# Kernel tuning notes

Measured on AMD Instinct MI355X. Metric: run time of the kernel, lower is better.

## Reference

```python
import jax, jax.numpy as jnp
import numpy as np

H, W, D = 200, 200, 16          # voxel grid dims
GRID = 0.4                       # voxel size (m)
MULT = 3.0                       # scale_multiplier (3-sigma radius)
PC_MIN = np.array([-40.0, -40.0, -1.0], dtype=np.float32)
B, N, M, C = 1, 16384, 4096, 18  # batch, query points, gaussians, semantic classes


def setup_inputs() -> dict:
    key = jax.random.key(0)
    ks = jax.random.split(key, 6)
    extent = jnp.array([H, W, D], dtype=jnp.float32) * GRID
    pc_min = jnp.asarray(PC_MIN)
    # points / means strictly inside the grid so int-voxel asserts hold
    pts = pc_min + jax.random.uniform(ks[0], (B, N, 3), dtype=jnp.float32) * (extent - 1e-3)
    means3D = pc_min + jax.random.uniform(ks[1], (B, M, 3), dtype=jnp.float32) * (extent - 1e-3)
    opacities = jax.random.uniform(ks[2], (B, M), dtype=jnp.float32, minval=0.1, maxval=1.0)
    semantics = jax.random.normal(ks[3], (B, M, C), dtype=jnp.float32)
    # scales chosen so ceil(max_scale*3/0.4) >= 1 (radii assert)
    scales = jax.random.uniform(ks[4], (B, M, 3), dtype=jnp.float32, minval=0.15, maxval=0.6)
    # SPD covariance per Gaussian: diag(scales^2) + small PSD perturbation
    Bm = 0.05 * jax.random.normal(ks[5], (B, M, 3, 3), dtype=jnp.float32)
    cov3D = jnp.eye(3, dtype=jnp.float32) * (scales ** 2)[..., :, None] + Bm @ jnp.swapaxes(Bm, -1, -2)
    return {"pts": pts, "means3D": means3D, "opacities": opacities,
            "semantics": semantics, "scales": scales, "cov3D": cov3D}


def _aggregate(pts_i, means_i, op_i, sem_i, sc_i, cov_i):
    # pts_i [N,3], means_i [M,3], op_i [M], sem_i [M,C], sc_i [M,3], cov_i [M,3,3]
    pc_min = jnp.asarray(PC_MIN)
    pint = jnp.floor((pts_i - pc_min) / GRID).astype(jnp.int32)    # [N,3] voxel of each point
    mint = jnp.floor((means_i - pc_min) / GRID).astype(jnp.int32)  # [M,3] voxel of each gaussian
    radii = jnp.ceil(jnp.max(sc_i, axis=-1) * MULT / GRID).astype(jnp.int32)  # [M] voxel radius
    A = jnp.linalg.inv(cov_i)                                       # [M,3,3] conic (inverse cov)
    Am = jnp.einsum('gij,gj->gi', A, means_i)                       # [M,3]
    mAm = jnp.einsum('gi,gi->g', means_i, Am)                       # [M]
    # Mahalanobis q[n,g] = (p-m)^T A (p-m) = p^T A p - 2 p^T A m + m^T A m, via [N,9]x[9,M] GEMM
    pp = (pts_i[:, :, None] * pts_i[:, None, :]).reshape(-1, 9)     # [N,9]
    pAp = pp @ A.reshape(-1, 9).T                                   # [N,M]
    q = pAp - 2.0 * (pts_i @ Am.T) + mAm[None, :]                   # [N,M]
    # gaussian contributes to a point iff the point's voxel lies in the gaussian's radius box
    mask = jnp.all(jnp.abs(pint[:, None, :] - mint[None, :, :]) <= radii[None, :, None], axis=-1)
    w = jnp.where(mask, jnp.exp(-0.5 * q) * op_i[None, :], 0.0)     # [N,M]
    return w @ sem_i                                                # [N,C] logits


def reference(pts, means3D, opacities, semantics, scales, cov3D):
    return jax.vmap(_aggregate)(pts, means3D, opacities, semantics, scales, cov3D)
```

## Files before the change

### kernel.cpp

```cpp
#include <hip/hip_runtime.h>

namespace {
constexpr float GRIDSZ = 0.4f;
constexpr float PCXY = -40.0f;
constexpr float PCZ  = -1.0f;
constexpr int CCH = 18;
constexpr int CELLS_X = 25;
constexpr int NCELLS = CELLS_X * CELLS_X;
constexpr int VMAX = 199;
constexpr int PCAP = 128;
constexpr int GCAP = 128;
constexpr int SEMW = 20;
}

__global__ __launch_bounds__(256) void prep_kernel(
    const float* __restrict__ pts, const float* __restrict__ means,
    const float* __restrict__ scales,
    unsigned short* __restrict__ pcell, unsigned* __restrict__ gcb,
    int N, int M) {
  int id = blockIdx.x * 256 + threadIdx.x;
  if (id < M) {
    int g = id;
    float mx = means[(size_t)g * 3 + 0], my = means[(size_t)g * 3 + 1];
    int mvx = (int)floorf((mx - PCXY) / GRIDSZ);
    int mvy = (int)floorf((my - PCXY) / GRIDSZ);
    float smax = fmaxf(scales[(size_t)g * 3 + 0],
                 fmaxf(scales[(size_t)g * 3 + 1], scales[(size_t)g * 3 + 2]));
    int r = (int)ceilf(smax * 3.0f / GRIDSZ);
    int cx0 = max(mvx - r, 0) >> 3, cx1 = min(mvx + r, VMAX) >> 3;
    int cy0 = max(mvy - r, 0) >> 3, cy1 = min(mvy + r, VMAX) >> 3;
    gcb[g] = (unsigned)cx0 | ((unsigned)cx1 << 8) | ((unsigned)cy0 << 16) | ((unsigned)cy1 << 24);
  } else if (id < M + N) {
    int p = id - M;
    float px = pts[(size_t)p * 3 + 0], py = pts[(size_t)p * 3 + 1];
    int pvx = (int)floorf((px - PCXY) / GRIDSZ);
    int pvy = (int)floorf((py - PCXY) / GRIDSZ);
    pcell[p] = (unsigned short)((pvx >> 3) + CELLS_X * (pvy >> 3));
  }
}

__global__ __launch_bounds__(256) void agg_kernel(
    const float* __restrict__ pts, const float* __restrict__ means,
    const float* __restrict__ opac, const float* __restrict__ scales,
    const float* __restrict__ cov, const float* __restrict__ sem,
    const unsigned short* __restrict__ pcell, const unsigned* __restrict__ gcb,
    float* __restrict__ out, int N, int M) {
  __shared__ int pcnt_s, gcnt_s;
  __shared__ int lpi[PCAP];
  __shared__ int lvox[PCAP];
  __shared__ float4 lpts[PCAP];
  __shared__ int graw[GCAP];
  __shared__ int gsrt[GCAP];
  __shared__ int4 lbox[GCAP];
  __shared__ float4 lpay[GCAP * 3];
  __shared__ float lsem[GCAP * SEMW];
  __shared__ float buf[3][64][CCH + 1];

  const int tid = threadIdx.x, lane = tid & 63, wave = tid >> 6;
  const unsigned cellv = blockIdx.x;
  const int cx = (int)(cellv % CELLS_X), cy = (int)(cellv / CELLS_X);

  if (tid == 0) { pcnt_s = 0; gcnt_s = 0; }
  __syncthreads();

  {
    const uint4* pc4 = reinterpret_cast<const uint4*>(pcell);
    const int n8 = N >> 3;
    for (int i8 = tid; i8 < n8; i8 += 256) {
      uint4 v = pc4[i8];
      unsigned w[4] = {v.x, v.y, v.z, v.w};
#pragma unroll
      for (int k = 0; k < 4; ++k) {
        if ((w[k] & 0xFFFFu) == cellv) {
          int s = atomicAdd(&pcnt_s, 1);
          if (s < PCAP) lpi[s] = i8 * 8 + 2 * k;
        }
        if ((w[k] >> 16) == cellv) {
          int s = atomicAdd(&pcnt_s, 1);
          if (s < PCAP) lpi[s] = i8 * 8 + 2 * k + 1;
        }
      }
    }
    for (int i = (n8 << 3) + tid; i < N; i += 256) {
      if (pcell[i] == cellv) {
        int s = atomicAdd(&pcnt_s, 1);
        if (s < PCAP) lpi[s] = i;
      }
    }
  }
  {
    const uint4* gb4 = reinterpret_cast<const uint4*>(gcb);
    const int m4 = M >> 2;
    for (int i4 = tid; i4 < m4; i4 += 256) {
      uint4 v = gb4[i4];
      unsigned gk[4] = {v.x, v.y, v.z, v.w};
#pragma unroll
      for (int k = 0; k < 4; ++k) {
        unsigned pk = gk[k];
        bool hit = (cx >= (int)(pk & 255u)) & (cx <= (int)((pk >> 8) & 255u)) &
                   (cy >= (int)((pk >> 16) & 255u)) & (cy <= (int)(pk >> 24));
        if (hit) {
          int s = atomicAdd(&gcnt_s, 1);
          if (s < GCAP) graw[s] = i4 * 4 + k;
        }
      }
    }
    for (int g = (m4 << 2) + tid; g < M; g += 256) {
      unsigned pk = gcb[g];
      bool hit = (cx >= (int)(pk & 255u)) & (cx <= (int)((pk >> 8) & 255u)) &
                 (cy >= (int)((pk >> 16) & 255u)) & (cy <= (int)(pk >> 24));
      if (hit) {
        int s = atomicAdd(&gcnt_s, 1);
        if (s < GCAP) graw[s] = g;
      }
    }
  }
  __syncthreads();
  const int P = min(pcnt_s, PCAP);
  const int K = min(gcnt_s, GCAP);

  if (tid < K) {
    int v = graw[tid], rank = 0;
    for (int j = 0; j < K; ++j) rank += (graw[j] < v);
    gsrt[rank] = v;
  }
  __syncthreads();

  if (tid < P) {
    int i = lpi[tid];
    float px = pts[(size_t)i * 3], py = pts[(size_t)i * 3 + 1], pz = pts[(size_t)i * 3 + 2];
    int pvx = (int)floorf((px - PCXY) / GRIDSZ);
    int pvy = (int)floorf((py - PCXY) / GRIDSZ);
    int pvz = (int)floorf((pz - PCZ) / GRIDSZ);
    lvox[tid] = pvx | (pvy << 8) | (pvz << 16);
    lpts[tid] = make_float4(px, py, pz, __int_as_float(i));
  } else if (tid >= 128 && tid - 128 < K) {
    int t = tid - 128;
    int g = gsrt[t];
    float mx = means[(size_t)g * 3], my = means[(size_t)g * 3 + 1], mz = means[(size_t)g * 3 + 2];
    int mvx = (int)floorf((mx - PCXY) / GRIDSZ);
    int mvy = (int)floorf((my - PCXY) / GRIDSZ);
    int mvz = (int)floorf((mz - PCZ) / GRIDSZ);
    float sm = fmaxf(scales[(size_t)g * 3],
               fmaxf(scales[(size_t)g * 3 + 1], scales[(size_t)g * 3 + 2]));
    int r = (int)ceilf(sm * 3.0f / GRIDSZ);
    lbox[t] = make_int4(mvx - r, mvy - r, mvz - r, 2 * r);
    const float* c = cov + (size_t)g * 9;
    float c00 = c[0], c01 = c[1], c02 = c[2], c11 = c[4], c12 = c[5], c22 = c[8];
    float M00 = c11 * c22 - c12 * c12;
    float M01 = c02 * c12 - c01 * c22;
    float M02 = c01 * c12 - c02 * c11;
    float inv = 1.0f / (c00 * M00 + c01 * M01 + c02 * M02);
    lpay[t * 3 + 0] = make_float4(mx, my, mz, opac[g]);
    lpay[t * 3 + 1] = make_float4(M00 * inv, M01 * inv, M02 * inv,
                                  (c00 * c22 - c02 * c02) * inv);
    lpay[t * 3 + 2] = make_float4((c01 * c02 - c00 * c12) * inv,
                                  (c00 * c11 - c01 * c01) * inv, 0.f, 0.f);
  }
  for (int idx = tid; idx < K * CCH; idx += 256) {
    int j = idx / CCH, c2 = idx - j * CCH;
    lsem[j * SEMW + c2] = sem[(size_t)gsrt[j] * CCH + c2];
  }
  __syncthreads();

  const int kq = (K + 3) >> 2;
  const int j0 = wave * kq, j1 = min(K, j0 + kq);

  for (int pb = 0; pb < P; pb += 64) {
    const bool vp = (pb + lane) < P;
    const float4 pt = lpts[vp ? pb + lane : 0];
    const int pv = vp ? lvox[pb + lane] : 0;
    int pvx = vp ? (pv & 255) : -100000;
    int pvy = (pv >> 8) & 255;
    int pvz = pv >> 16;

    float acc[CCH];
#pragma unroll
    for (int c = 0; c < CCH; ++c) acc[c] = 0.f;

    for (int j = j0; j < j1; ++j) {
      int4 bx = lbox[j];
      bool m = ((unsigned)(pvx - bx.x) <= (unsigned)bx.w) &
               ((unsigned)(pvy - bx.y) <= (unsigned)bx.w) &
               ((unsigned)(pvz - bx.z) <= (unsigned)bx.w);
      if (__any(m)) {
        float4 q0 = lpay[j * 3 + 0];
        float4 q1 = lpay[j * 3 + 1];
        float4 q2 = lpay[j * 3 + 2];
        float dx = pt.x - q0.x, dy = pt.y - q0.y, dz = pt.z - q0.z;
        float t0 = q1.x * dx + q1.y * dy + q1.z * dz;
        float t1 = q1.y * dx + q1.w * dy + q2.x * dz;
        float t2 = q1.z * dx + q2.x * dy + q2.y * dz;
        float qq = dx * t0 + dy * t1 + dz * t2;
        float w = m ? __expf(-0.5f * qq) * q0.w : 0.f;
        const float4* s4 = reinterpret_cast<const float4*>(&lsem[j * SEMW]);
        float4 sa = s4[0], sb = s4[1], sc = s4[2], sd = s4[3];
        float2 se = *reinterpret_cast<const float2*>(&lsem[j * SEMW + 16]);
        acc[0]  = fmaf(w, sa.x, acc[0]);  acc[1]  = fmaf(w, sa.y, acc[1]);
        acc[2]  = fmaf(w, sa.z, acc[2]);  acc[3]  = fmaf(w, sa.w, acc[3]);
        acc[4]  = fmaf(w, sb.x, acc[4]);  acc[5]  = fmaf(w, sb.y, acc[5]);
        acc[6]  = fmaf(w, sb.z, acc[6]);  acc[7]  = fmaf(w, sb.w, acc[7]);
        acc[8]  = fmaf(w, sc.x, acc[8]);  acc[9]  = fmaf(w, sc.y, acc[9]);
        acc[10] = fmaf(w, sc.z, acc[10]); acc[11] = fmaf(w, sc.w, acc[11]);
        acc[12] = fmaf(w, sd.x, acc[12]); acc[13] = fmaf(w, sd.y, acc[13]);
        acc[14] = fmaf(w, sd.z, acc[14]); acc[15] = fmaf(w, sd.w, acc[15]);
        acc[16] = fmaf(w, se.x, acc[16]); acc[17] = fmaf(w, se.y, acc[17]);
      }
    }

    if (wave > 0) {
#pragma unroll
      for (int c = 0; c < CCH; ++c) buf[wave - 1][lane][c] = acc[c];
    }
    __syncthreads();
    if (wave == 0 && vp) {
      int myp = __float_as_int(pt.w);
      float* o = out + (size_t)myp * CCH;
#pragma unroll
      for (int c = 0; c < CCH; ++c)
        o[c] = acc[c] + buf[0][lane][c] + buf[1][lane][c] + buf[2][lane][c];
    }
    __syncthreads();
  }
}

extern "C" void kernel_launch(void* const* d_in, const int* in_sizes, int n_in,
                              void* d_out, int out_size, void* d_ws, size_t ws_size,
                              hipStream_t stream) {
  const float* pts     = (const float*)d_in[0];
  const float* means3D = (const float*)d_in[1];
  const float* opac    = (const float*)d_in[2];
  const float* sem     = (const float*)d_in[3];
  const float* scales  = (const float*)d_in[4];
  const float* cov3D   = (const float*)d_in[5];
  float* out = (float*)d_out;

  int N = in_sizes[0] / 3;
  int M = in_sizes[1] / 3;

  char* ws = (char*)d_ws;
  size_t off = 0;
  auto alloc = [&](size_t bytes) { char* p = ws + off; off = (off + bytes + 255) & ~(size_t)255; return p; };
  unsigned short* pcell = (unsigned short*)alloc((size_t)N * 2);
  unsigned*       gcb   = (unsigned*)alloc((size_t)M * 4);

  prep_kernel<<<(N + M + 255) / 256, 256, 0, stream>>>(
      pts, means3D, scales, pcell, gcb, N, M);

  agg_kernel<<<NCELLS, 256, 0, stream>>>(
      pts, means3D, opac, scales, cov3D, sem, pcell, gcb, out, N, M);
}
```

Before: 22.17 us.

## Process two cells per block and pack gaussian cell boxes into 16 bits

Each aggregation block now handles two adjacent grid cells, so the full scans of point-cell and gaussian-box arrays are shared across two cells, halving redundant global scanning work. The gaussian cell-range descriptor is compressed from 32 to 16 bits (start plus small extent), halving that scan's bandwidth. The tradeoff is half as many blocks (313 vs 625), which lowers parallelism on a large GPU, and the per-cell compute phases run serially inside each block.

Result: slower. 27.19 us (+22.6%).

```diff
diff --git a/kernel.cpp b/kernel.cpp
--- a/kernel.cpp
+++ b/kernel.cpp
@@ -8,6 +8,8 @@
 constexpr int CELLS_X = 25;
 constexpr int NCELLS = CELLS_X * CELLS_X;
 constexpr int VMAX = 199;
+constexpr int BCELL = 2;
+constexpr int NBLK = (NCELLS + BCELL - 1) / BCELL;
 constexpr int PCAP = 128;
 constexpr int GCAP = 128;
 constexpr int SEMW = 20;
@@ -16,7 +18,7 @@
 __global__ __launch_bounds__(256) void prep_kernel(
     const float* __restrict__ pts, const float* __restrict__ means,
     const float* __restrict__ scales,
-    unsigned short* __restrict__ pcell, unsigned* __restrict__ gcb,
+    unsigned short* __restrict__ pcell, unsigned short* __restrict__ gcb,
     int N, int M) {
   int id = blockIdx.x * 256 + threadIdx.x;
   if (id < M) {
@@ -29,7 +31,8 @@
     int r = (int)ceilf(smax * 3.0f / GRIDSZ);
     int cx0 = max(mvx - r, 0) >> 3, cx1 = min(mvx + r, VMAX) >> 3;
     int cy0 = max(mvy - r, 0) >> 3, cy1 = min(mvy + r, VMAX) >> 3;
-    gcb[g] = (unsigned)cx0 | ((unsigned)cx1 << 8) | ((unsigned)cy0 << 16) | ((unsigned)cy1 << 24);
+    gcb[g] = (unsigned short)((unsigned)cx0 | ((unsigned)(cx1 - cx0) << 5) |
+                              ((unsigned)cy0 << 7) | ((unsigned)(cy1 - cy0) << 12));
   } else if (id < M + N) {
     int p = id - M;
     float px = pts[(size_t)p * 3 + 0], py = pts[(size_t)p * 3 + 1];
@@ -43,24 +46,27 @@
     const float* __restrict__ pts, const float* __restrict__ means,
     const float* __restrict__ opac, const float* __restrict__ scales,
     const float* __restrict__ cov, const float* __restrict__ sem,
-    const unsigned short* __restrict__ pcell, const unsigned* __restrict__ gcb,
+    const unsigned short* __restrict__ pcell, const unsigned short* __restrict__ gcb,
     float* __restrict__ out, int N, int M) {
-  __shared__ int pcnt_s, gcnt_s;
-  __shared__ int lpi[PCAP];
+  __shared__ int pcnt_s[BCELL], gcnt_s[BCELL];
+  __shared__ int lpi2[BCELL][PCAP];
+  __shared__ int graw2[BCELL][GCAP];
+  __shared__ int gsrt[GCAP];
   __shared__ int lvox[PCAP];
   __shared__ float4 lpts[PCAP];
-  __shared__ int graw[GCAP];
-  __shared__ int gsrt[GCAP];
   __shared__ int4 lbox[GCAP];
   __shared__ float4 lpay[GCAP * 3];
   __shared__ float lsem[GCAP * SEMW];
   __shared__ float buf[3][64][CCH + 1];
 
   const int tid = threadIdx.x, lane = tid & 63, wave = tid >> 6;
-  const unsigned cellv = blockIdx.x;
-  const int cx = (int)(cellv % CELLS_X), cy = (int)(cellv / CELLS_X);
-
-  if (tid == 0) { pcnt_s = 0; gcnt_s = 0; }
+  const unsigned c0 = blockIdx.x * BCELL;
+  const int cxA = (int)(c0 % CELLS_X), cyA = (int)(c0 / CELLS_X);
+  const bool has1 = (c0 + 1) < NCELLS;
+  const int cxB = has1 ? (int)((c0 + 1) % CELLS_X) : 255;
+  const int cyB = has1 ? (int)((c0 + 1) / CELLS_X) : 255;
+
+  if (tid < BCELL) { pcnt_s[tid] = 0; gcnt_s[tid] = 0; }
   __syncthreads();
 
   {
@@ -71,156 +77,177 @@
       unsigned w[4] = {v.x, v.y, v.z, v.w};
 #pragma unroll
       for (int k = 0; k < 4; ++k) {
-        if ((w[k] & 0xFFFFu) == cellv) {
-          int s = atomicAdd(&pcnt_s, 1);
-          if (s < PCAP) lpi[s] = i8 * 8 + 2 * k;
-        }
-        if ((w[k] >> 16) == cellv) {
-          int s = atomicAdd(&pcnt_s, 1);
-          if (s < PCAP) lpi[s] = i8 * 8 + 2 * k + 1;
+        unsigned dlo = (w[k] & 0xFFFFu) - c0;
+        if (dlo < (unsigned)BCELL) {
+          int s = atomicAdd(&pcnt_s[dlo], 1);
+          if (s < PCAP) lpi2[dlo][s] = i8 * 8 + 2 * k;
+        }
+        unsigned dhi = (w[k] >> 16) - c0;
+        if (dhi < (unsigned)BCELL) {
+          int s = atomicAdd(&pcnt_s[dhi], 1);
+          if (s < PCAP) lpi2[dhi][s] = i8 * 8 + 2 * k + 1;
         }
       }
     }
     for (int i = (n8 << 3) + tid; i < N; i += 256) {
-      if (pcell[i] == cellv) {
-        int s = atomicAdd(&pcnt_s, 1);
-        if (s < PCAP) lpi[s] = i;
+      unsigned d = (unsigned)pcell[i] - c0;
+      if (d < (unsigned)BCELL) {
+        int s = atomicAdd(&pcnt_s[d], 1);
+        if (s < PCAP) lpi2[d][s] = i;
       }
     }
   }
   {
     const uint4* gb4 = reinterpret_cast<const uint4*>(gcb);
-    const int m4 = M >> 2;
-    for (int i4 = tid; i4 < m4; i4 += 256) {
-      uint4 v = gb4[i4];
-      unsigned gk[4] = {v.x, v.y, v.z, v.w};
+    const int m8 = M >> 3;
+    for (int i8 = tid; i8 < m8; i8 += 256) {
+      uint4 v = gb4[i8];
+      unsigned w[4] = {v.x, v.y, v.z, v.w};
 #pragma unroll
       for (int k = 0; k < 4; ++k) {
-        unsigned pk = gk[k];
-        bool hit = (cx >= (int)(pk & 255u)) & (cx <= (int)((pk >> 8) & 255u)) &
-                   (cy >= (int)((pk >> 16) & 255u)) & (cy <= (int)(pk >> 24));
-        if (hit) {
-          int s = atomicAdd(&gcnt_s, 1);
-          if (s < GCAP) graw[s] = i4 * 4 + k;
-        }
-      }
-    }
-    for (int g = (m4 << 2) + tid; g < M; g += 256) {
-      unsigned pk = gcb[g];
-      bool hit = (cx >= (int)(pk & 255u)) & (cx <= (int)((pk >> 8) & 255u)) &
-                 (cy >= (int)((pk >> 16) & 255u)) & (cy <= (int)(pk >> 24));
-      if (hit) {
-        int s = atomicAdd(&gcnt_s, 1);
-        if (s < GCAP) graw[s] = g;
+#pragma unroll
+        for (int h = 0; h < 2; ++h) {
+          unsigned u = (h == 0) ? (w[k] & 0xFFFFu) : (w[k] >> 16);
+          int g = i8 * 8 + 2 * k + h;
+          int gx0 = (int)(u & 31u), dx = (int)((u >> 5) & 3u);
+          int gy0 = (int)((u >> 7) & 31u), dy = (int)((u >> 12) & 3u);
+          if (((unsigned)(cxA - gx0) <= (unsigned)dx) &
+              ((unsigned)(cyA - gy0) <= (unsigned)dy)) {
+            int s = atomicAdd(&gcnt_s[0], 1);
+            if (s < GCAP) graw2[0][s] = g;
+          }
+          if (((unsigned)(cxB - gx0) <= (unsigned)dx) &
+              ((unsigned)(cyB - gy0) <= (unsigned)dy)) {
+            int s = atomicAdd(&gcnt_s[1], 1);
+            if (s < GCAP) graw2[1][s] = g;
+          }
+        }
+      }
+    }
+    for (int g = (m8 << 3) + tid; g < M; g += 256) {
+      unsigned u = gcb[g];
+      int gx0 = (int)(u & 31u), dx = (int)((u >> 5) & 3u);
+      int gy0 = (int)((u >> 7) & 31u), dy = (int)((u >> 12) & 3u);
+      if (((unsigned)(cxA - gx0) <= (unsigned)dx) & ((unsigned)(cyA - gy0) <= (unsigned)dy)) {
+        int s = atomicAdd(&gcnt_s[0], 1);
+        if (s < GCAP) graw2[0][s] = g;
+      }
+      if (((unsigned)(cxB - gx0) <= (unsigned)dx) & ((unsigned)(cyB - gy0) <= (unsigned)dy)) {
+        int s = atomicAdd(&gcnt_s[1], 1);
+        if (s < GCAP) graw2[1][s] = g;
       }
     }
   }
   __syncthreads();
-  const int P = min(pcnt_s, PCAP);
-  const int K = min(gcnt_s, GCAP);
-
-  if (tid < K) {
-    int v = graw[tid], rank = 0;
-    for (int j = 0; j < K; ++j) rank += (graw[j] < v);
-    gsrt[rank] = v;
-  }
-  __syncthreads();
-
-  if (tid < P) {
-    int i = lpi[tid];
-    float px = pts[(size_t)i * 3], py = pts[(size_t)i * 3 + 1], pz = pts[(size_t)i * 3 + 2];
-    int pvx = (int)floorf((px - PCXY) / GRIDSZ);
-    int pvy = (int)floorf((py - PCXY) / GRIDSZ);
-    int pvz = (int)floorf((pz - PCZ) / GRIDSZ);
-    lvox[tid] = pvx | (pvy << 8) | (pvz << 16);
-    lpts[tid] = make_float4(px, py, pz, __int_as_float(i));
-  } else if (tid >= 128 && tid - 128 < K) {
-    int t = tid - 128;
-    int g = gsrt[t];
-    float mx = means[(size_t)g * 3], my = means[(size_t)g * 3 + 1], mz = means[(size_t)g * 3 + 2];
-    int mvx = (int)floorf((mx - PCXY) / GRIDSZ);
-    int mvy = (int)floorf((my - PCXY) / GRIDSZ);
-    int mvz = (int)floorf((mz - PCZ) / GRIDSZ);
-    float sm = fmaxf(scales[(size_t)g * 3],
-               fmaxf(scales[(size_t)g * 3 + 1], scales[(size_t)g * 3 + 2]));
-    int r = (int)ceilf(sm * 3.0f / GRIDSZ);
-    lbox[t] = make_int4(mvx - r, mvy - r, mvz - r, 2 * r);
-    const float* c = cov + (size_t)g * 9;
-    float c00 = c[0], c01 = c[1], c02 = c[2], c11 = c[4], c12 = c[5], c22 = c[8];
-    float M00 = c11 * c22 - c12 * c12;
-    float M01 = c02 * c12 - c01 * c22;
-    float M02 = c01 * c12 - c02 * c11;
-    float inv = 1.0f / (c00 * M00 + c01 * M01 + c02 * M02);
-    lpay[t * 3 + 0] = make_float4(mx, my, mz, opac[g]);
-    lpay[t * 3 + 1] = make_float4(M00 * inv, M01 * inv, M02 * inv,
-                                  (c00 * c22 - c02 * c02) * inv);
-    lpay[t * 3 + 2] = make_float4((c01 * c02 - c00 * c12) * inv,
-                                  (c00 * c11 - c01 * c01) * inv, 0.f, 0.f);
-  }
-  for (int idx = tid; idx < K * CCH; idx += 256) {
-    int j = idx / CCH, c2 = idx - j * CCH;
-    lsem[j * SEMW + c2] = sem[(size_t)gsrt[j] * CCH + c2];
-  }
-  __syncthreads();
-
-  const int kq = (K + 3) >> 2;
-  const int j0 = wave * kq, j1 = min(K, j0 + kq);
-
-  for (int pb = 0; pb < P; pb += 64) {
-    const bool vp = (pb + lane) < P;
-    const float4 pt = lpts[vp ? pb + lane : 0];
-    const int pv = vp ? lvox[pb + lane] : 0;
-    int pvx = vp ? (pv & 255) : -100000;
-    int pvy = (pv >> 8) & 255;
-    int pvz = pv >> 16;
-
-    float acc[CCH];
-#pragma unroll
-    for (int c = 0; c < CCH; ++c) acc[c] = 0.f;
-
-    for (int j = j0; j < j1; ++j) {
-      int4 bx = lbox[j];
-      bool m = ((unsigned)(pvx - bx.x) <= (unsigned)bx.w) &
-               ((unsigned)(pvy - bx.y) <= (unsigned)bx.w) &
-               ((unsigned)(pvz - bx.z) <= (unsigned)bx.w);
-      if (__any(m)) {
-        float4 q0 = lpay[j * 3 + 0];
-        float4 q1 = lpay[j * 3 + 1];
-        float4 q2 = lpay[j * 3 + 2];
-        float dx = pt.x - q0.x, dy = pt.y - q0.y, dz = pt.z - q0.z;
-        float t0 = q1.x * dx + q1.y * dy + q1.z * dz;
-        float t1 = q1.y * dx + q1.w * dy + q2.x * dz;
-        float t2 = q1.z * dx + q2.x * dy + q2.y * dz;
-        float qq = dx * t0 + dy * t1 + dz * t2;
-        float w = m ? __expf(-0.5f * qq) * q0.w : 0.f;
-        const float4* s4 = reinterpret_cast<const float4*>(&lsem[j * SEMW]);
-        float4 sa = s4[0], sb = s4[1], sc = s4[2], sd = s4[3];
-        float2 se = *reinterpret_cast<const float2*>(&lsem[j * SEMW + 16]);
-        acc[0]  = fmaf(w, sa.x, acc[0]);  acc[1]  = fmaf(w, sa.y, acc[1]);
-        acc[2]  = fmaf(w, sa.z, acc[2]);  acc[3]  = fmaf(w, sa.w, acc[3]);
-        acc[4]  = fmaf(w, sb.x, acc[4]);  acc[5]  = fmaf(w, sb.y, acc[5]);
-        acc[6]  = fmaf(w, sb.z, acc[6]);  acc[7]  = fmaf(w, sb.w, acc[7]);
-        acc[8]  = fmaf(w, sc.x, acc[8]);  acc[9]  = fmaf(w, sc.y, acc[9]);
-        acc[10] = fmaf(w, sc.z, acc[10]); acc[11] = fmaf(w, sc.w, acc[11]);
-        acc[12] = fmaf(w, sd.x, acc[12]); acc[13] = fmaf(w, sd.y, acc[13]);
-        acc[14] = fmaf(w, sd.z, acc[14]); acc[15] = fmaf(w, sd.w, acc[15]);
-        acc[16] = fmaf(w, se.x, acc[16]); acc[17] = fmaf(w, se.y, acc[17]);
-      }
-    }
-
-    if (wave > 0) {
-#pragma unroll
-      for (int c = 0; c < CCH; ++c) buf[wave - 1][lane][c] = acc[c];
+
+  const int ncc = has1 ? BCELL : 1;
+  for (int cc = 0; cc < ncc; ++cc) {
+    const int P = min(pcnt_s[cc], PCAP);
+    const int K = min(gcnt_s[cc], GCAP);
+
+    if (tid < K) {
+      int v = graw2[cc][tid], rank = 0;
+      for (int j = 0; j < K; ++j) rank += (graw2[cc][j] < v);
+      gsrt[rank] = v;
     }
     __syncthreads();
-    if (wave == 0 && vp) {
-      int myp = __float_as_int(pt.w);
-      float* o = out + (size_t)myp * CCH;
-#pragma unroll
-      for (int c = 0; c < CCH; ++c)
-        o[c] = acc[c] + buf[0][lane][c] + buf[1][lane][c] + buf[2][lane][c];
+
+    if (tid < P) {
+      int i = lpi2[cc][tid];
+      float px = pts[(size_t)i * 3], py = pts[(size_t)i * 3 + 1], pz = pts[(size_t)i * 3 + 2];
+      int pvx = (int)floorf((px - PCXY) / GRIDSZ);
+      int pvy = (int)floorf((py - PCXY) / GRIDSZ);
+      int pvz = (int)floorf((pz - PCZ) / GRIDSZ);
+      lvox[tid] = pvx | (pvy << 8) | (pvz << 16);
+      lpts[tid] = make_float4(px, py, pz, __int_as_float(i));
+    } else if (tid >= 128 && tid - 128 < K) {
+      int t = tid - 128;
+      int g = gsrt[t];
+      float mx = means[(size_t)g * 3], my = means[(size_t)g * 3 + 1], mz = means[(size_t)g * 3 + 2];
+      int mvx = (int)floorf((mx - PCXY) / GRIDSZ);
+      int mvy = (int)floorf((my - PCXY) / GRIDSZ);
+      int mvz = (int)floorf((mz - PCZ) / GRIDSZ);
+      float sm = fmaxf(scales[(size_t)g * 3],
+                 fmaxf(scales[(size_t)g * 3 + 1], scales[(size_t)g * 3 + 2]));
+      int r = (int)ceilf(sm * 3.0f / GRIDSZ);
+      lbox[t] = make_int4(mvx - r, mvy - r, mvz - r, 2 * r);
+      const float* c = cov + (size_t)g * 9;
+      float c00 = c[0], c01 = c[1], c02 = c[2], c11 = c[4], c12 = c[5], c22 = c[8];
+      float M00 = c11 * c22 - c12 * c12;
+      float M01 = c02 * c12 - c01 * c22;
+      float M02 = c01 * c12 - c02 * c11;
+      float inv = 1.0f / (c00 * M00 + c01 * M01 + c02 * M02);
+      lpay[t * 3 + 0] = make_float4(mx, my, mz, opac[g]);
+      lpay[t * 3 + 1] = make_float4(M00 * inv, M01 * inv, M02 * inv,
+                                    (c00 * c22 - c02 * c02) * inv);
+      lpay[t * 3 + 2] = make_float4((c01 * c02 - c00 * c12) * inv,
+                                    (c00 * c11 - c01 * c01) * inv, 0.f, 0.f);
+    }
+    for (int idx = tid; idx < K * CCH; idx += 256) {
+      int j = idx / CCH, c2 = idx - j * CCH;
+      lsem[j * SEMW + c2] = sem[(size_t)gsrt[j] * CCH + c2];
     }
     __syncthreads();
+
+    const int kq = (K + 3) >> 2;
+    const int j0 = wave * kq, j1 = min(K, j0 + kq);
+
+    for (int pb = 0; pb < P; pb += 64) {
+      const bool vp = (pb + lane) < P;
+      const float4 pt = lpts[vp ? pb + lane : 0];
+      const int pv = vp ? lvox[pb + lane] : 0;
+      int pvx = vp ? (pv & 255) : -100000;
+      int pvy = (pv >> 8) & 255;
+      int pvz = pv >> 16;
+
+      float acc[CCH];
+#pragma unroll
+      for (int c = 0; c < CCH; ++c) acc[c] = 0.f;
+
+      for (int j = j0; j < j1; ++j) {
+        int4 bx = lbox[j];
+        bool m = ((unsigned)(pvx - bx.x) <= (unsigned)bx.w) &
+                 ((unsigned)(pvy - bx.y) <= (unsigned)bx.w) &
+                 ((unsigned)(pvz - bx.z) <= (unsigned)bx.w);
+        if (__any(m)) {
+          float4 q0 = lpay[j * 3 + 0];
+          float4 q1 = lpay[j * 3 + 1];
+          float4 q2 = lpay[j * 3 + 2];
+          float dx = pt.x - q0.x, dy = pt.y - q0.y, dz = pt.z - q0.z;
+          float t0 = q1.x * dx + q1.y * dy + q1.z * dz;
+          float t1 = q1.y * dx + q1.w * dy + q2.x * dz;
+          float t2 = q1.z * dx + q2.x * dy + q2.y * dz;
+          float qq = dx * t0 + dy * t1 + dz * t2;
+          float w = m ? __expf(-0.5f * qq) * q0.w : 0.f;
+          const float4* s4 = reinterpret_cast<const float4*>(&lsem[j * SEMW]);
+          float4 sa = s4[0], sb = s4[1], sc = s4[2], sd = s4[3];
+          float2 se = *reinterpret_cast<const float2*>(&lsem[j * SEMW + 16]);
+          acc[0]  = fmaf(w, sa.x, acc[0]);  acc[1]  = fmaf(w, sa.y, acc[1]);
+          acc[2]  = fmaf(w, sa.z, acc[2]);  acc[3]  = fmaf(w, sa.w, acc[3]);
+          acc[4]  = fmaf(w, sb.x, acc[4]);  acc[5]  = fmaf(w, sb.y, acc[5]);
+          acc[6]  = fmaf(w, sb.z, acc[6]);  acc[7]  = fmaf(w, sb.w, acc[7]);
+          acc[8]  = fmaf(w, sc.x, acc[8]);  acc[9]  = fmaf(w, sc.y, acc[9]);
+          acc[10] = fmaf(w, sc.z, acc[10]); acc[11] = fmaf(w, sc.w, acc[11]);
+          acc[12] = fmaf(w, sd.x, acc[12]); acc[13] = fmaf(w, sd.y, acc[13]);
+          acc[14] = fmaf(w, sd.z, acc[14]); acc[15] = fmaf(w, sd.w, acc[15]);
+          acc[16] = fmaf(w, se.x, acc[16]); acc[17] = fmaf(w, se.y, acc[17]);
+        }
+      }
+
+      if (wave > 0) {
+#pragma unroll
+        for (int c = 0; c < CCH; ++c) buf[wave - 1][lane][c] = acc[c];
+      }
+      __syncthreads();
+      if (wave == 0 && vp) {
+        int myp = __float_as_int(pt.w);
+        float* o = out + (size_t)myp * CCH;
+#pragma unroll
+        for (int c = 0; c < CCH; ++c)
+          o[c] = acc[c] + buf[0][lane][c] + buf[1][lane][c] + buf[2][lane][c];
+      }
+      __syncthreads();
+    }
   }
 }
 
@@ -242,11 +269,11 @@
   size_t off = 0;
   auto alloc = [&](size_t bytes) { char* p = ws + off; off = (off + bytes + 255) & ~(size_t)255; return p; };
   unsigned short* pcell = (unsigned short*)alloc((size_t)N * 2);
-  unsigned*       gcb   = (unsigned*)alloc((size_t)M * 4);
+  unsigned short* gcb   = (unsigned short*)alloc((size_t)M * 2);
 
   prep_kernel<<<(N + M + 255) / 256, 256, 0, stream>>>(
       pts, means3D, scales, pcell, gcb, N, M);
 
-  agg_kernel<<<NCELLS, 256, 0, stream>>>(
+  agg_kernel<<<NBLK, 256, 0, stream>>>(
       pts, means3D, opac, scales, cov3D, sem, pcell, gcb, out, N, M);
 }
```
